# Performance work log

Hardware: AMD Instinct MI355X
Metric: run time of the kernel (lower is better)

## Reference

```python
import jax, jax.numpy as jnp
import numpy as np
import math

D_MODEL = 1024
N_HEADS = 16
D_HEAD = D_MODEL // N_HEADS
B, T = 2, 2048


def setup_inputs() -> dict:
    key = jax.random.key(0)
    ks = jax.random.split(key, 10)
    H = jax.random.normal(ks[0], (B, T, D_MODEL), dtype=jnp.float32)
    key_padding_mask = jnp.zeros((B, T), dtype=bool)
    s = 0.02
    Wq = jax.random.normal(ks[1], (D_MODEL, D_MODEL), dtype=jnp.float32) * s
    bq = jnp.zeros((D_MODEL,), dtype=jnp.float32)
    Wk = jax.random.normal(ks[2], (D_MODEL, D_MODEL), dtype=jnp.float32) * s
    bk = jnp.zeros((D_MODEL,), dtype=jnp.float32)
    Wv = jax.random.normal(ks[3], (D_MODEL, D_MODEL), dtype=jnp.float32) * s
    bv = jnp.zeros((D_MODEL,), dtype=jnp.float32)
    Wo = jax.random.normal(ks[4], (D_MODEL, D_MODEL), dtype=jnp.float32) * s
    bo = jnp.zeros((D_MODEL,), dtype=jnp.float32)
    return {"H": H, "key_padding_mask": key_padding_mask,
            "Wq": Wq, "bq": bq, "Wk": Wk, "bk": bk,
            "Wv": Wv, "bv": bv, "Wo": Wo, "bo": bo}


def _heads(x):
    # [B, T, D] -> [B, nh, T, dh]
    b, t, _ = x.shape
    return x.reshape(b, t, N_HEADS, D_HEAD).transpose(0, 2, 1, 3)


def reference(H, key_padding_mask, Wq, bq, Wk, bk, Wv, bv, Wo, bo):
    b, t, d = H.shape
    q = _heads(H @ Wq.T + bq)
    k = _heads(H @ Wk.T + bk)
    v = _heads(H @ Wv.T + bv)
    scale = 1.0 / math.sqrt(D_HEAD)
    scores = jnp.einsum("bhqd,bhkd->bhqk", q, k) * scale
    # causal: add (mask - 1) * 1e9, as in the torch module (soft -1e9, not -inf)
    idx = jnp.arange(t)
    causal_mask = (idx[None, :] <= idx[:, None]).astype(scores.dtype)
    scores = scores + (causal_mask[None, None, :, :] - 1.0) * 1e9
    # key padding mask: True = masked -> -inf
    scores = jnp.where(key_padding_mask[:, None, None, :], -jnp.inf, scores)
    A = jax.nn.softmax(scores, axis=-1)
    O = jnp.einsum("bhqk,bhkd->bhqd", A, v)
    O = O.transpose(0, 2, 1, 3).reshape(b, t, d)
    return O @ Wo.T + bo
```

## Files before the change

### kernel.cpp

```cpp
#include <hip/hip_runtime.h>
#include <hip/hip_bf16.h>


typedef __bf16 bf16x8 __attribute__((ext_vector_type(8)));
typedef float  f32x4  __attribute__((ext_vector_type(4)));
typedef unsigned short u16x4 __attribute__((ext_vector_type(4)));

#define AS1 __attribute__((address_space(1)))
#define AS3 __attribute__((address_space(3)))

__device__ __forceinline__ void gll16(const void* g, void* l) {
  __builtin_amdgcn_global_load_lds((const AS1 void*)g, (AS3 void*)l, 16, 0, 0);
}

__device__ __forceinline__ unsigned short f2bf(float x) {
  unsigned u = __builtin_bit_cast(unsigned, x);
  u += 0x7fffu + ((u >> 16) & 1u);
  return (unsigned short)(u >> 16);
}

__device__ __forceinline__ unsigned cvtpk(float lo, float hi) {
  unsigned r;
  asm("v_cvt_pk_bf16_f32 %0, %1, %2" : "=v"(r) : "v"(lo), "v"(hi));
  return r;
}

__global__ __launch_bounds__(256) void cvt_kernel(
    const float* __restrict__ H,  const float* __restrict__ Wq,
    const float* __restrict__ Wk, const float* __restrict__ Wv,
    const float* __restrict__ Wo,
    unsigned short* __restrict__ Hb, unsigned short* __restrict__ Wcat,
    unsigned short* __restrict__ Wob)
{
  size_t i = ((size_t)blockIdx.x * 256 + threadIdx.x) * 4;
  const float* s; unsigned short* d;
  if      (i < 4194304u) { s = H  + i;            d = Hb   + i; }
  else if (i < 5242880u) { s = Wq + (i - 4194304); d = Wcat + (i - 4194304); }
  else if (i < 6291456u) { s = Wk + (i - 5242880); d = Wcat + (i - 4194304); }
  else if (i < 7340032u) { s = Wv + (i - 6291456); d = Wcat + (i - 4194304); }
  else                   { s = Wo + (i - 7340032); d = Wob  + (i - 7340032); }
  f32x4 v = *(const f32x4*)s;
  u16x4 o;
  o[0] = f2bf(v[0]); o[1] = f2bf(v[1]); o[2] = f2bf(v[2]); o[3] = f2bf(v[3]);
  *(u16x4*)d = o;
}

__global__ __launch_bounds__(512, 2) void gemm_qkv(
    const unsigned short* __restrict__ A,
    const unsigned short* __restrict__ B,
    const float* __restrict__ b0, const float* __restrict__ b1,
    const float* __restrict__ b2,
    unsigned short* __restrict__ Qb, unsigned short* __restrict__ Kb,
    unsigned short* __restrict__ Vt)
{
  constexpr int K = 1024, NT = 32;
  __shared__ __align__(1024) char smem[131072];
  const int tid = threadIdx.x;
  const int w = tid >> 6, l = tid & 63;
  const int lr = l & 15, lg = l >> 4;
  const int wn = w & 3, wm = w >> 2;

  const int bid = blockIdx.x;
  const int xcd = bid & 7, idx = bid >> 3;
  const int by = (xcd & 3) * 8 + (idx & 7);
  const int bx = (xcd >> 2) * 4 + (idx >> 3);

  const unsigned short* srcB =
      (w < 6) ? B + (size_t)(bx*384 + w*64 + lr) * K + lg*8
              : A + (size_t)(by*128 + (w-6)*64 + lr) * K + lg*8;

  auto stage = [&](int t) {
    const int ring = t & 3;
    const unsigned short* s = srcB + t*32;
    char* d = smem + ring*32768 + w*4096;
#pragma unroll
    for (int i = 0; i < 4; ++i)
      gll16(s + (size_t)i*16*K, d + i*1024);
  };

  f32x4 acc[6][4] = {};

  stage(0); stage(1); stage(2);
  asm volatile("s_waitcnt vmcnt(8)" ::: "memory");
  __builtin_amdgcn_s_barrier();

  for (int t = 0; t < NT; ++t) {
    const char* Wt = smem + (t&3)*32768 + wn*6144;
    const char* Ht = smem + (t&3)*32768 + 24576 + wm*4096;
    bf16x8 wf[6], hf[4];
#pragma unroll
    for (int p = 0; p < 6; ++p)
      wf[p] = *(const bf16x8*)(Wt + p*1024 + l*16);
#pragma unroll
    for (int q = 0; q < 4; ++q)
      hf[q] = *(const bf16x8*)(Ht + q*1024 + l*16);
    if (t + 3 < NT) stage(t + 3);
    __builtin_amdgcn_s_setprio(1);
#pragma unroll
    for (int p = 0; p < 6; ++p)
#pragma unroll
      for (int q = 0; q < 4; ++q)
        acc[p][q] = __builtin_amdgcn_mfma_f32_16x16x32_bf16(wf[p], hf[q], acc[p][q], 0, 0, 0);
    __builtin_amdgcn_s_setprio(0);
    if (t + 3 < NT)      asm volatile("s_waitcnt vmcnt(8)" ::: "memory");
    else if (t + 2 < NT) asm volatile("s_waitcnt vmcnt(4)" ::: "memory");
    else if (t + 1 < NT) asm volatile("s_waitcnt vmcnt(0)" ::: "memory");
    if (t + 1 < NT) __builtin_amdgcn_s_barrier();
  }

  constexpr float CS = 0.125f * 1.44269504088896340736f;
#pragma unroll
  for (int p = 0; p < 6; ++p) {
    const int nG = bx*384 + wn*96 + p*16 + lg*4;
    const int sel = nG >> 10, nl = nG & 1023, h = nl >> 6, dd = nl & 63;
    const float sc = (sel == 0) ? CS : 1.0f;
    const float* bp = (sel == 0) ? b0 : ((sel == 1) ? b1 : b2);
    const f32x4 bias = *(const f32x4*)(bp + nl);
#pragma unroll
    for (int q = 0; q < 4; ++q) {
      const int m = by*128 + wm*64 + q*16 + lr;
      const int bb = m >> 11, tt = m & 2047;
      if (sel < 2) {
        unsigned short* O = sel ? Kb : Qb;
        u16x4 pk;
#pragma unroll
        for (int r = 0; r < 4; ++r) pk[r] = f2bf((acc[p][q][r] + bias[r]) * sc);
        *(u16x4*)(O + ((size_t)(bb*16 + h) * 2048 + tt) * 64 + dd) = pk;
      } else {
#pragma unroll
        for (int r = 0; r < 4; ++r)
          Vt[((size_t)(bb*16 + h) * 64 + dd + r) * 2048 + tt] =
              f2bf(acc[p][q][r] + bias[r]);
      }
    }
  }
}

__global__ __launch_bounds__(512) void gemm_o(
    const unsigned short* __restrict__ A,
    const unsigned short* __restrict__ B,
    float* __restrict__ Cout, const float* __restrict__ bo)
{
  constexpr int K = 1024, NT = 16;
  __shared__ __align__(1024) char smem[81920];
  const int tid = threadIdx.x;
  const int w = tid >> 6, l = tid & 63;
  const int lr = l & 15, lg = l >> 4;
  const int wn = w >> 1, wm = w & 1;

  const int bid = blockIdx.x;
  const int xcd = bid & 7, idx = bid >> 3;
  const int by = xcd * 4 + (idx & 3);
  const int bx = idx >> 2;

  const unsigned short* srcW = B + (size_t)(bx*128 + w*16 + lr) * K + lg*8;
  const unsigned short* srcH = A + (size_t)(by*128 + w*16 + lr) * K + lg*8;

  auto stW = [&](int t) {
    const unsigned short* s = srcW + t*64;
    char* d = smem + (t&1)*16384 + w*2048;
    gll16(s,      d);
    gll16(s + 32, d + 1024);
  };
  auto stH = [&](int t, int ring) {
    const unsigned short* s = srcH + t*64;
    char* d = smem + 32768 + ring*16384 + w*2048;
    gll16(s,      d);
    gll16(s + 32, d + 1024);
  };

  f32x4 acc[2][4] = {};

  stW(0); stH(0, 0); stH(1, 1);
  asm volatile("s_waitcnt vmcnt(2)" ::: "memory");
  __builtin_amdgcn_s_barrier();

  auto tile = [&](int t, int r0, int r2) {
    const char* Wt = smem + (t&1)*16384 + wn*4096;
    const char* Ht = smem + 32768 + r0*16384 + wm*8192;
    bf16x8 wf[2][2], hfa[2][2], hfb[2][2];
#pragma unroll
    for (int p = 0; p < 2; ++p)
#pragma unroll
      for (int kf = 0; kf < 2; ++kf)
        wf[p][kf] = *(const bf16x8*)(Wt + (p*2+kf)*1024 + l*16);
#pragma unroll
    for (int q = 0; q < 2; ++q)
#pragma unroll
      for (int kf = 0; kf < 2; ++kf)
        hfa[q][kf] = *(const bf16x8*)(Ht + (q*2+kf)*1024 + l*16);
    if (t+1 < NT) stW(t+1);
    __builtin_amdgcn_s_barrier();
    __builtin_amdgcn_s_setprio(1);
#pragma unroll
    for (int p = 0; p < 2; ++p)
#pragma unroll
      for (int q = 0; q < 2; ++q)
#pragma unroll
        for (int kf = 0; kf < 2; ++kf)
          acc[p][q] = __builtin_amdgcn_mfma_f32_16x16x32_bf16(wf[p][kf], hfa[q][kf], acc[p][q], 0, 0, 0);
    __builtin_amdgcn_s_setprio(0);
    __builtin_amdgcn_s_barrier();
#pragma unroll
    for (int q = 0; q < 2; ++q)
#pragma unroll
      for (int kf = 0; kf < 2; ++kf)
        hfb[q][kf] = *(const bf16x8*)(Ht + ((q+2)*2+kf)*1024 + l*16);
    if (t+2 < NT) stH(t+2, r2);
    __builtin_amdgcn_s_barrier();
    __builtin_amdgcn_s_setprio(1);
#pragma unroll
    for (int p = 0; p < 2; ++p)
#pragma unroll
      for (int q = 0; q < 2; ++q)
#pragma unroll
        for (int kf = 0; kf < 2; ++kf)
          acc[p][q+2] = __builtin_amdgcn_mfma_f32_16x16x32_bf16(wf[p][kf], hfb[q][kf], acc[p][q+2], 0, 0, 0);
    __builtin_amdgcn_s_setprio(0);
    if (t+2 < NT)      asm volatile("s_waitcnt vmcnt(2)" ::: "memory");
    else if (t+1 < NT) asm volatile("s_waitcnt vmcnt(0)" ::: "memory");
    __builtin_amdgcn_s_barrier();
  };

  int r0 = 0;
  for (int t = 0; t < NT; ++t) {
    int r2 = r0 + 2; if (r2 >= 3) r2 -= 3;
    tile(t, r0, r2);
    ++r0; if (r0 == 3) r0 = 0;
  }

  __syncthreads();
#pragma unroll
  for (int p = 0; p < 2; ++p) {
    const int n0 = wn*32 + p*16 + lg*4;
    const f32x4 bias = *(const f32x4*)(bo + bx*128 + n0);
#pragma unroll
    for (int q = 0; q < 4; ++q) {
      const int m = wm*64 + q*16 + lr;
      *(f32x4*)(smem + m*528 + n0*4) = acc[p][q] + bias;
    }
  }
  __syncthreads();
#pragma unroll
  for (int pass = 0; pass < 8; ++pass) {
    const int m = pass*16 + (tid >> 5), c = tid & 31;
    f32x4 v = *(const f32x4*)(smem + m*528 + c*16);
    *(f32x4*)(Cout + (size_t)(by*128 + m) * 1024 + bx*128 + c*4) = v;
  }
}

__global__ __launch_bounds__(256, 2) void attn_kernel(
    const unsigned short* __restrict__ Qb, const unsigned short* __restrict__ Kb,
    const unsigned short* __restrict__ Vt, unsigned short* __restrict__ AO)
{
  __shared__ char smem[3*16384 + 4*2304];
  const int tid = threadIdx.x;
  const int w  = tid >> 6, l = tid & 63;
  const int lr = l & 15,  lg = l >> 4;
  const int bid = blockIdx.x;
  const int xcd = bid & 7, idx = bid >> 3;
  const int bh = xcd + ((idx & 3) << 3);
  const int pr = idx >> 2;
  const int qtA = pr, qtB = 31 - pr;
  const size_t bh_off = (size_t)bh * 2048 * 64;
  const unsigned short* Qp = Qb + bh_off;
  const unsigned short* Kp = Kb + bh_off;
  const unsigned short* Vp = Vt + bh_off;
  const int qwA = qtA*64 + w*16, qwB = qtB*64 + w*16;

  bf16x8 qfA[2], qfB[2];
#pragma unroll
  for (int kf = 0; kf < 2; ++kf) {
    qfA[kf] = *(const bf16x8*)(Qp + (size_t)(qwA + lr) * 64 + kf*32 + lg*8);
    qfB[kf] = *(const bf16x8*)(Qp + (size_t)(qwB + lr) * 64 + kf*32 + lg*8);
  }

  f32x4 accA[4] = {}, accB[4] = {};
  float mA = -3e38f, lA = 0.f, mB = -3e38f, lB = 0.f;
  char* Pw = smem + 49152 + w * 2304;

  const int nt = qtB + 1;

  auto stage = [&](int t, int b) {
#pragma unroll
    for (int i = 0; i < 2; ++i) {
      const int c = w * 2 + i;
      const int sub = c >> 1, kf = c & 1;
      const int kv0 = t * 64;
      gll16(Kp + (size_t)(kv0 + sub*16 + lr) * 64 + kf*32 + lg*8,
            smem + b * 16384 + c * 1024);
      gll16(Vp + (size_t)(sub*16 + lr) * 2048 + kv0 + kf*32 + lg*8,
            smem + b * 16384 + 8192 + c * 1024);
    }
  };

  auto process = [&](const bf16x8 (&qf)[2], f32x4 (&acc_o)[4], float& m_run,
                     float& l_run, int qw, bool diag, int kv0, int buf) {
    f32x4 accs[4] = {};
    __builtin_amdgcn_s_setprio(1);
#pragma unroll
    for (int kf = 0; kf < 2; ++kf)
#pragma unroll
      for (int kt = 0; kt < 4; ++kt) {
        bf16x8 kfr = *(const bf16x8*)(smem + buf*16384 + (kt*2 + kf)*1024 + l*16);
        accs[kt] = __builtin_amdgcn_mfma_f32_16x16x32_bf16(kfr, qf[kf], accs[kt], 0, 0, 0);
      }
    __builtin_amdgcn_s_setprio(0);

    float s[4][4];
    const int qg = qw + lr;
#pragma unroll
    for (int kt = 0; kt < 4; ++kt)
#pragma unroll
      for (int r = 0; r < 4; ++r) {
        float v = accs[kt][r];
        if (diag) {
          const int kvg = kv0 + kt*16 + lg*4 + r;
          if (kvg > qg) v = -1e30f;
        }
        s[kt][r] = v;
      }

    float mt = s[0][0];
#pragma unroll
    for (int kt = 0; kt < 4; ++kt)
#pragma unroll
      for (int r = 0; r < 4; ++r) mt = fmaxf(mt, s[kt][r]);
    mt = fmaxf(mt, __shfl_xor(mt, 16));
    mt = fmaxf(mt, __shfl_xor(mt, 32));

    if (__any(mt > m_run + 8.f)) {
      const float mnew = fmaxf(m_run, mt);
      const float fac  = __builtin_amdgcn_exp2f(m_run - mnew);
      l_run *= fac;
#pragma unroll
      for (int r = 0; r < 4; ++r) {
        const float fr = __shfl(fac, lg*4 + r);
#pragma unroll
        for (int dt = 0; dt < 4; ++dt) acc_o[dt][r] *= fr;
      }
      m_run = mnew;
    }

    float p[4][4]; float sum = 0.f;
#pragma unroll
    for (int kt = 0; kt < 4; ++kt)
#pragma unroll
      for (int r = 0; r < 4; ++r) {
        const float e = __builtin_amdgcn_exp2f(s[kt][r] - m_run);
        p[kt][r] = e; sum += e;
      }
    sum += __shfl_xor(sum, 16);
    sum += __shfl_xor(sum, 32);
    l_run += sum;

#pragma unroll
    for (int kt = 0; kt < 4; ++kt)
#pragma unroll
      for (int r2 = 0; r2 < 2; ++r2)
        *(unsigned*)(Pw + lr*144 + (kt*16 + lg*4 + r2*2)*2) =
            cvtpk(p[kt][r2*2], p[kt][r2*2+1]);

    __builtin_amdgcn_s_setprio(1);
#pragma unroll
    for (int kf2 = 0; kf2 < 2; ++kf2) {
      bf16x8 pf = *(const bf16x8*)(Pw + lr*144 + kf2*64 + lg*16);
#pragma unroll
      for (int dt = 0; dt < 4; ++dt) {
        bf16x8 vf = *(const bf16x8*)(smem + buf*16384 + 8192 + (dt*2 + kf2)*1024 + l*16);
        acc_o[dt] = __builtin_amdgcn_mfma_f32_16x16x32_bf16(pf, vf, acc_o[dt], 0, 0, 0);
      }
    }
    __builtin_amdgcn_s_setprio(0);
  };

  stage(0, 0); stage(1, 1);
  asm volatile("s_waitcnt vmcnt(4)" ::: "memory");
  __builtin_amdgcn_s_barrier();

  int bcur = 0;
  for (int t = 0; t < nt; ++t) {
    if (t + 2 < nt) {
      int b2 = bcur + 2; if (b2 >= 3) b2 -= 3;
      stage(t + 2, b2);
    }
    process(qfB, accB, mB, lB, qwB, t == qtB, t*64, bcur);
    if (t <= qtA)
      process(qfA, accA, mA, lA, qwA, t == qtA, t*64, bcur);
    if (t + 2 < nt)      asm volatile("s_waitcnt vmcnt(4)" ::: "memory");
    else if (t + 1 < nt) asm volatile("s_waitcnt vmcnt(0)" ::: "memory");
    if (t + 1 < nt) __builtin_amdgcn_s_barrier();
    ++bcur; if (bcur == 3) bcur = 0;
  }

  const int b_ = bh >> 4, h = bh & 15;
#pragma unroll
  for (int r = 0; r < 4; ++r) {
    const float linvB = 1.0f / __shfl(lB, lg*4 + r);
    const int tgB = qwB + lg*4 + r;
    const size_t baseB = ((size_t)(b_*2048 + tgB)) * 1024 + h*64 + lr;
#pragma unroll
    for (int dt = 0; dt < 4; ++dt)
      AO[baseB + dt*16] = f2bf(accB[dt][r] * linvB);
    const float linvA = 1.0f / __shfl(lA, lg*4 + r);
    const int tgA = qwA + lg*4 + r;
    const size_t baseA = ((size_t)(b_*2048 + tgA)) * 1024 + h*64 + lr;
#pragma unroll
    for (int dt = 0; dt < 4; ++dt)
      AO[baseA + dt*16] = f2bf(accA[dt][r] * linvA);
  }
}

extern "C" void kernel_launch(void* const* d_in, const int* in_sizes, int n_in,
                              void* d_out, int out_size, void* d_ws, size_t ws_size,
                              hipStream_t stream) {
  const float* H  = (const float*)d_in[0];
  const float* Wq = (const float*)d_in[2];
  const float* bq = (const float*)d_in[3];
  const float* Wk = (const float*)d_in[4];
  const float* bk = (const float*)d_in[5];
  const float* Wv = (const float*)d_in[6];
  const float* bv = (const float*)d_in[7];
  const float* Wo = (const float*)d_in[8];
  const float* bo = (const float*)d_in[9];

  char* ws = (char*)d_ws;
  unsigned short* Hb   = (unsigned short*)(ws);
  unsigned short* Wcat = (unsigned short*)(ws + 8388608);
  unsigned short* Wob  = (unsigned short*)(ws + 14680064);
  unsigned short* Qb   = (unsigned short*)(ws + 16777216);
  unsigned short* Kb   = (unsigned short*)(ws + 25165824);
  unsigned short* Vt   = (unsigned short*)(ws + 33554432);
  unsigned short* AOb  = (unsigned short*)(ws + 41943040);

  cvt_kernel<<<8192, 256, 0, stream>>>(H, Wq, Wk, Wv, Wo, Hb, Wcat, Wob);
  gemm_qkv<<<256, 512, 0, stream>>>(Hb, Wcat, bq, bk, bv, Qb, Kb, Vt);
  attn_kernel<<<512, 256, 0, stream>>>(Qb, Kb, Vt, AOb);
  gemm_o<<<256, 512, 0, stream>>>(AOb, Wob, (float*)d_out, bo);
}
```

Baseline: 111.7 us.

## Interleave both query tiles' attention steps into one dual-tile pass

While both query tiles are still active, the attention loop now handles them in one interleaved routine. It issues their QK and PV MFMAs side by side from the same K/V fragment loads, and runs their softmax steps together. Each tile gets its own P staging buffer in LDS, so shared memory per block grows. The aim is to cut duplicate LDS reads and give the scheduler more independent work to hide MFMA and exp latency. The cost is higher register pressure under the existing launch bounds, which could cause spills.

```diff
diff --git a/kernel.cpp b/kernel.cpp
--- a/kernel.cpp
+++ b/kernel.cpp
@@ -253,7 +253,7 @@
     const unsigned short* __restrict__ Qb, const unsigned short* __restrict__ Kb,
     const unsigned short* __restrict__ Vt, unsigned short* __restrict__ AO)
 {
-  __shared__ char smem[3*16384 + 4*2304];
+  __shared__ char smem[3*16384 + 8*2304];
   const int tid = threadIdx.x;
   const int w  = tid >> 6, l = tid & 63;
   const int lr = l & 15,  lg = l >> 4;
@@ -277,7 +277,8 @@
 
   f32x4 accA[4] = {}, accB[4] = {};
   float mA = -3e38f, lA = 0.f, mB = -3e38f, lB = 0.f;
-  char* Pw = smem + 49152 + w * 2304;
+  char* PwB = smem + 49152 + w * 2304;
+  char* PwA = smem + 49152 + (w + 4) * 2304;
 
   const int nt = qtB + 1;
 
@@ -294,8 +295,7 @@
     }
   };
 
-  auto process = [&](const bf16x8 (&qf)[2], f32x4 (&acc_o)[4], float& m_run,
-                     float& l_run, int qw, bool diag, int kv0, int buf) {
+  auto process = [&](bool diag, int kv0, int buf) {
     f32x4 accs[4] = {};
     __builtin_amdgcn_s_setprio(1);
 #pragma unroll
@@ -303,12 +303,12 @@
 #pragma unroll
       for (int kt = 0; kt < 4; ++kt) {
         bf16x8 kfr = *(const bf16x8*)(smem + buf*16384 + (kt*2 + kf)*1024 + l*16);
-        accs[kt] = __builtin_amdgcn_mfma_f32_16x16x32_bf16(kfr, qf[kf], accs[kt], 0, 0, 0);
+        accs[kt] = __builtin_amdgcn_mfma_f32_16x16x32_bf16(kfr, qfB[kf], accs[kt], 0, 0, 0);
       }
     __builtin_amdgcn_s_setprio(0);
 
     float s[4][4];
-    const int qg = qw + lr;
+    const int qg = qwB + lr;
 #pragma unroll
     for (int kt = 0; kt < 4; ++kt)
 #pragma unroll
@@ -329,17 +329,17 @@
     mt = fmaxf(mt, __shfl_xor(mt, 16));
     mt = fmaxf(mt, __shfl_xor(mt, 32));
 
-    if (__any(mt > m_run + 8.f)) {
-      const float mnew = fmaxf(m_run, mt);
-      const float fac  = __builtin_amdgcn_exp2f(m_run - mnew);
-      l_run *= fac;
+    if (__any(mt > mB + 8.f)) {
+      const float mnew = fmaxf(mB, mt);
+      const float fac  = __builtin_amdgcn_exp2f(mB - mnew);
+      lB *= fac;
 #pragma unroll
       for (int r = 0; r < 4; ++r) {
         const float fr = __shfl(fac, lg*4 + r);
 #pragma unroll
-        for (int dt = 0; dt < 4; ++dt) acc_o[dt][r] *= fr;
-      }
-      m_run = mnew;
+        for (int dt = 0; dt < 4; ++dt) accB[dt][r] *= fr;
+      }
+      mB = mnew;
     }
 
     float p[4][4]; float sum = 0.f;
@@ -347,28 +347,135 @@
     for (int kt = 0; kt < 4; ++kt)
 #pragma unroll
       for (int r = 0; r < 4; ++r) {
-        const float e = __builtin_amdgcn_exp2f(s[kt][r] - m_run);
+        const float e = __builtin_amdgcn_exp2f(s[kt][r] - mB);
         p[kt][r] = e; sum += e;
       }
     sum += __shfl_xor(sum, 16);
     sum += __shfl_xor(sum, 32);
-    l_run += sum;
+    lB += sum;
 
 #pragma unroll
     for (int kt = 0; kt < 4; ++kt)
 #pragma unroll
       for (int r2 = 0; r2 < 2; ++r2)
-        *(unsigned*)(Pw + lr*144 + (kt*16 + lg*4 + r2*2)*2) =
+        *(unsigned*)(PwB + lr*144 + (kt*16 + lg*4 + r2*2)*2) =
             cvtpk(p[kt][r2*2], p[kt][r2*2+1]);
 
     __builtin_amdgcn_s_setprio(1);
 #pragma unroll
     for (int kf2 = 0; kf2 < 2; ++kf2) {
-      bf16x8 pf = *(const bf16x8*)(Pw + lr*144 + kf2*64 + lg*16);
+      bf16x8 pf = *(const bf16x8*)(PwB + lr*144 + kf2*64 + lg*16);
 #pragma unroll
       for (int dt = 0; dt < 4; ++dt) {
         bf16x8 vf = *(const bf16x8*)(smem + buf*16384 + 8192 + (dt*2 + kf2)*1024 + l*16);
-        acc_o[dt] = __builtin_amdgcn_mfma_f32_16x16x32_bf16(pf, vf, acc_o[dt], 0, 0, 0);
+        accB[dt] = __builtin_amdgcn_mfma_f32_16x16x32_bf16(pf, vf, accB[dt], 0, 0, 0);
+      }
+    }
+    __builtin_amdgcn_s_setprio(0);
+  };
+
+  auto processDual = [&](bool diagA, int kv0, int buf) {
+    f32x4 accsB[4] = {}, accsA[4] = {};
+    __builtin_amdgcn_s_setprio(1);
+#pragma unroll
+    for (int kf = 0; kf < 2; ++kf)
+#pragma unroll
+      for (int kt = 0; kt < 4; ++kt) {
+        bf16x8 kfr = *(const bf16x8*)(smem + buf*16384 + (kt*2 + kf)*1024 + l*16);
+        accsB[kt] = __builtin_amdgcn_mfma_f32_16x16x32_bf16(kfr, qfB[kf], accsB[kt], 0, 0, 0);
+        accsA[kt] = __builtin_amdgcn_mfma_f32_16x16x32_bf16(kfr, qfA[kf], accsA[kt], 0, 0, 0);
+      }
+    __builtin_amdgcn_s_setprio(0);
+
+    float sB[4][4], sA[4][4];
+    const int qgA = qwA + lr;
+#pragma unroll
+    for (int kt = 0; kt < 4; ++kt)
+#pragma unroll
+      for (int r = 0; r < 4; ++r) {
+        sB[kt][r] = accsB[kt][r];
+        float v = accsA[kt][r];
+        if (diagA) {
+          const int kvg = kv0 + kt*16 + lg*4 + r;
+          if (kvg > qgA) v = -1e30f;
+        }
+        sA[kt][r] = v;
+      }
+
+    float mtB = sB[0][0], mtA = sA[0][0];
+#pragma unroll
+    for (int kt = 0; kt < 4; ++kt)
+#pragma unroll
+      for (int r = 0; r < 4; ++r) {
+        mtB = fmaxf(mtB, sB[kt][r]);
+        mtA = fmaxf(mtA, sA[kt][r]);
+      }
+    mtB = fmaxf(mtB, __shfl_xor(mtB, 16));
+    mtA = fmaxf(mtA, __shfl_xor(mtA, 16));
+    mtB = fmaxf(mtB, __shfl_xor(mtB, 32));
+    mtA = fmaxf(mtA, __shfl_xor(mtA, 32));
+
+    if (__any(mtB > mB + 8.f)) {
+      const float mnew = fmaxf(mB, mtB);
+      const float fac  = __builtin_amdgcn_exp2f(mB - mnew);
+      lB *= fac;
+#pragma unroll
+      for (int r = 0; r < 4; ++r) {
+        const float fr = __shfl(fac, lg*4 + r);
+#pragma unroll
+        for (int dt = 0; dt < 4; ++dt) accB[dt][r] *= fr;
+      }
+      mB = mnew;
+    }
+    if (__any(mtA > mA + 8.f)) {
+      const float mnew = fmaxf(mA, mtA);
+      const float fac  = __builtin_amdgcn_exp2f(mA - mnew);
+      lA *= fac;
+#pragma unroll
+      for (int r = 0; r < 4; ++r) {
+        const float fr = __shfl(fac, lg*4 + r);
+#pragma unroll
+        for (int dt = 0; dt < 4; ++dt) accA[dt][r] *= fr;
+      }
+      mA = mnew;
+    }
+
+    float pB[4][4], pA[4][4]; float sumB = 0.f, sumA = 0.f;
+#pragma unroll
+    for (int kt = 0; kt < 4; ++kt)
+#pragma unroll
+      for (int r = 0; r < 4; ++r) {
+        const float eB = __builtin_amdgcn_exp2f(sB[kt][r] - mB);
+        const float eA = __builtin_amdgcn_exp2f(sA[kt][r] - mA);
+        pB[kt][r] = eB; sumB += eB;
+        pA[kt][r] = eA; sumA += eA;
+      }
+    sumB += __shfl_xor(sumB, 16);
+    sumA += __shfl_xor(sumA, 16);
+    sumB += __shfl_xor(sumB, 32);
+    sumA += __shfl_xor(sumA, 32);
+    lB += sumB; lA += sumA;
+
+#pragma unroll
+    for (int kt = 0; kt < 4; ++kt)
+#pragma unroll
+      for (int r2 = 0; r2 < 2; ++r2) {
+        *(unsigned*)(PwB + lr*144 + (kt*16 + lg*4 + r2*2)*2) =
+            cvtpk(pB[kt][r2*2], pB[kt][r2*2+1]);
+        *(unsigned*)(PwA + lr*144 + (kt*16 + lg*4 + r2*2)*2) =
+            cvtpk(pA[kt][r2*2], pA[kt][r2*2+1]);
+      }
+
+    __builtin_amdgcn_s_setprio(1);
+#pragma unroll
+    for (int kf2 = 0; kf2 < 2; ++kf2) {
+      bf16x8 pfB = *(const bf16x8*)(PwB + lr*144 + kf2*64 + lg*16);
+      bf16x8 pfA = *(const bf16x8*)(PwA + lr*144 + kf2*64 + lg*16);
+#pragma unroll
+      for (int dt = 0; dt < 4; ++dt) {
+        bf16x8 vf = *(const bf16x8*)(smem + buf*16384 + 8192 + (dt*2 + kf2)*1024 + l*16);
+        accB[dt] = __builtin_amdgcn_mfma_f32_16x16x32_bf16(pfB, vf, accB[dt], 0, 0, 0);
+        accA[dt] = __builtin_amdgcn_mfma_f32_16x16x32_bf16(pfA, vf, accA[dt], 0, 0, 0);
       }
     }
     __builtin_amdgcn_s_setprio(0);
@@ -384,9 +491,8 @@
       int b2 = bcur + 2; if (b2 >= 3) b2 -= 3;
       stage(t + 2, b2);
     }
-    process(qfB, accB, mB, lB, qwB, t == qtB, t*64, bcur);
-    if (t <= qtA)
-      process(qfA, accA, mA, lA, qwA, t == qtA, t*64, bcur);
+    if (t <= qtA) processDual(t == qtA, t*64, bcur);
+    else          process(t == qtB, t*64, bcur);
     if (t + 2 < nt)      asm volatile("s_waitcnt vmcnt(4)" ::: "memory");
     else if (t + 1 < nt) asm volatile("s_waitcnt vmcnt(0)" ::: "memory");
     if (t + 1 < nt) __builtin_amdgcn_s_barrier();
```

Result: no change. 112.1 us (+0.3%).

## Use 128-wide KV tiles with shared K fragments for both query tiles

Applied to the files above, without the earlier changes.

The attention loop now processes 128 keys per iteration instead of 64, moving from a triple-buffered to a double-buffered LDS schedule. Each K fragment read from LDS feeds the QK^T MFMAs of both paired query tiles, and the causal mask is applied only on the diagonal tile. The P staging buffer uses an XOR swizzle to cut LDS bank conflicts. The aim is fewer barriers and loop iterations and less LDS read traffic, at the cost of more LDS per block, higher register pressure, and less prefetch depth.

```diff
diff --git a/kernel.cpp b/kernel.cpp
--- a/kernel.cpp
+++ b/kernel.cpp
@@ -253,7 +253,7 @@
     const unsigned short* __restrict__ Qb, const unsigned short* __restrict__ Kb,
     const unsigned short* __restrict__ Vt, unsigned short* __restrict__ AO)
 {
-  __shared__ char smem[3*16384 + 4*2304];
+  __shared__ char smem[2*32768 + 4*4096];
   const int tid = threadIdx.x;
   const int w  = tid >> 6, l = tid & 63;
   const int lr = l & 15,  lg = l >> 4;
@@ -277,55 +277,32 @@
 
   f32x4 accA[4] = {}, accB[4] = {};
   float mA = -3e38f, lA = 0.f, mB = -3e38f, lB = 0.f;
-  char* Pw = smem + 49152 + w * 2304;
-
-  const int nt = qtB + 1;
+  char* Pw = smem + 65536 + w * 4096;
+  const int xr = (lr & 7) << 4;
+
+  const int nt = (qtB >> 1) + 1;
+  const int dualEnd = qtA >> 1;
 
   auto stage = [&](int t, int b) {
 #pragma unroll
-    for (int i = 0; i < 2; ++i) {
-      const int c = w * 2 + i;
-      const int sub = c >> 1, kf = c & 1;
-      const int kv0 = t * 64;
-      gll16(Kp + (size_t)(kv0 + sub*16 + lr) * 64 + kf*32 + lg*8,
-            smem + b * 16384 + c * 1024);
-      gll16(Vp + (size_t)(sub*16 + lr) * 2048 + kv0 + kf*32 + lg*8,
-            smem + b * 16384 + 8192 + c * 1024);
-    }
-  };
-
-  auto process = [&](const bf16x8 (&qf)[2], f32x4 (&acc_o)[4], float& m_run,
-                     float& l_run, int qw, bool diag, int kv0, int buf) {
-    f32x4 accs[4] = {};
-    __builtin_amdgcn_s_setprio(1);
-#pragma unroll
-    for (int kf = 0; kf < 2; ++kf)
-#pragma unroll
-      for (int kt = 0; kt < 4; ++kt) {
-        bf16x8 kfr = *(const bf16x8*)(smem + buf*16384 + (kt*2 + kf)*1024 + l*16);
-        accs[kt] = __builtin_amdgcn_mfma_f32_16x16x32_bf16(kfr, qf[kf], accs[kt], 0, 0, 0);
-      }
-    __builtin_amdgcn_s_setprio(0);
-
-    float s[4][4];
-    const int qg = qw + lr;
-#pragma unroll
-    for (int kt = 0; kt < 4; ++kt)
-#pragma unroll
-      for (int r = 0; r < 4; ++r) {
-        float v = accs[kt][r];
-        if (diag) {
-          const int kvg = kv0 + kt*16 + lg*4 + r;
-          if (kvg > qg) v = -1e30f;
-        }
-        s[kt][r] = v;
-      }
-
-    float mt = s[0][0];
-#pragma unroll
-    for (int kt = 0; kt < 4; ++kt)
-#pragma unroll
-      for (int r = 0; r < 4; ++r) mt = fmaxf(mt, s[kt][r]);
+    for (int i = 0; i < 4; ++i) {
+      const int c = w*4 + i;
+      const int kt = c >> 1, kf = c & 1;
+      gll16(Kp + (size_t)(t*128 + kt*16 + lr) * 64 + kf*32 + lg*8,
+            smem + b*32768 + c*1024);
+      const int dt = c >> 2, kf2 = c & 3;
+      gll16(Vp + (size_t)(dt*16 + lr) * 2048 + t*128 + kf2*32 + lg*8,
+            smem + b*32768 + 16384 + c*1024);
+    }
+  };
+
+  auto finish = [&](f32x4 (&a)[8], f32x4 (&acc_o)[4], float& m_run,
+                    float& l_run, int buf) {
+    float mt = a[0][0];
+#pragma unroll
+    for (int kt = 0; kt < 8; ++kt)
+#pragma unroll
+      for (int r = 0; r < 4; ++r) mt = fmaxf(mt, a[kt][r]);
     mt = fmaxf(mt, __shfl_xor(mt, 16));
     mt = fmaxf(mt, __shfl_xor(mt, 32));
 
@@ -342,55 +319,92 @@
       m_run = mnew;
     }
 
-    float p[4][4]; float sum = 0.f;
-#pragma unroll
-    for (int kt = 0; kt < 4; ++kt)
+    float sum = 0.f;
+#pragma unroll
+    for (int kt = 0; kt < 8; ++kt)
 #pragma unroll
       for (int r = 0; r < 4; ++r) {
-        const float e = __builtin_amdgcn_exp2f(s[kt][r] - m_run);
-        p[kt][r] = e; sum += e;
+        const float e = __builtin_amdgcn_exp2f(a[kt][r] - m_run);
+        a[kt][r] = e; sum += e;
       }
     sum += __shfl_xor(sum, 16);
     sum += __shfl_xor(sum, 32);
     l_run += sum;
 
 #pragma unroll
-    for (int kt = 0; kt < 4; ++kt)
+    for (int kt = 0; kt < 8; ++kt)
 #pragma unroll
       for (int r2 = 0; r2 < 2; ++r2)
-        *(unsigned*)(Pw + lr*144 + (kt*16 + lg*4 + r2*2)*2) =
-            cvtpk(p[kt][r2*2], p[kt][r2*2+1]);
+        *(unsigned*)(Pw + lr*256 + ((kt*32 + lg*8 + r2*4) ^ xr)) =
+            cvtpk(a[kt][r2*2], a[kt][r2*2+1]);
 
     __builtin_amdgcn_s_setprio(1);
 #pragma unroll
-    for (int kf2 = 0; kf2 < 2; ++kf2) {
-      bf16x8 pf = *(const bf16x8*)(Pw + lr*144 + kf2*64 + lg*16);
+    for (int kf2 = 0; kf2 < 4; ++kf2) {
+      bf16x8 pf = *(const bf16x8*)(Pw + lr*256 + ((kf2*64 + lg*16) ^ xr));
 #pragma unroll
       for (int dt = 0; dt < 4; ++dt) {
-        bf16x8 vf = *(const bf16x8*)(smem + buf*16384 + 8192 + (dt*2 + kf2)*1024 + l*16);
+        bf16x8 vf = *(const bf16x8*)(smem + buf*32768 + 16384 + (dt*4 + kf2)*1024 + l*16);
         acc_o[dt] = __builtin_amdgcn_mfma_f32_16x16x32_bf16(pf, vf, acc_o[dt], 0, 0, 0);
       }
     }
     __builtin_amdgcn_s_setprio(0);
   };
 
-  stage(0, 0); stage(1, 1);
-  asm volatile("s_waitcnt vmcnt(4)" ::: "memory");
+  auto maskDiag = [&](f32x4 (&a)[8], int qg, int kv0) {
+#pragma unroll
+    for (int kt = 0; kt < 8; ++kt)
+#pragma unroll
+      for (int r = 0; r < 4; ++r) {
+        const int kvg = kv0 + kt*16 + lg*4 + r;
+        if (kvg > qg) a[kt][r] = -1e30f;
+      }
+  };
+
+  stage(0, 0);
+  asm volatile("s_waitcnt vmcnt(0)" ::: "memory");
   __builtin_amdgcn_s_barrier();
 
-  int bcur = 0;
+  int cur = 0;
   for (int t = 0; t < nt; ++t) {
-    if (t + 2 < nt) {
-      int b2 = bcur + 2; if (b2 >= 3) b2 -= 3;
-      stage(t + 2, b2);
-    }
-    process(qfB, accB, mB, lB, qwB, t == qtB, t*64, bcur);
-    if (t <= qtA)
-      process(qfA, accA, mA, lA, qwA, t == qtA, t*64, bcur);
-    if (t + 2 < nt)      asm volatile("s_waitcnt vmcnt(4)" ::: "memory");
-    else if (t + 1 < nt) asm volatile("s_waitcnt vmcnt(0)" ::: "memory");
-    if (t + 1 < nt) __builtin_amdgcn_s_barrier();
-    ++bcur; if (bcur == 3) bcur = 0;
+    if (t + 1 < nt) stage(t + 1, cur ^ 1);
+    const int kv0 = t * 128;
+
+    if (t <= dualEnd) {
+      f32x4 aB[8] = {}, aA[8] = {};
+      __builtin_amdgcn_s_setprio(1);
+#pragma unroll
+      for (int kf = 0; kf < 2; ++kf)
+#pragma unroll
+        for (int kt = 0; kt < 8; ++kt) {
+          bf16x8 kfr = *(const bf16x8*)(smem + cur*32768 + (kt*2 + kf)*1024 + l*16);
+          aB[kt] = __builtin_amdgcn_mfma_f32_16x16x32_bf16(kfr, qfB[kf], aB[kt], 0, 0, 0);
+          aA[kt] = __builtin_amdgcn_mfma_f32_16x16x32_bf16(kfr, qfA[kf], aA[kt], 0, 0, 0);
+        }
+      __builtin_amdgcn_s_setprio(0);
+      if (t == dualEnd) maskDiag(aA, qwA + lr, kv0);
+      finish(aB, accB, mB, lB, cur);
+      finish(aA, accA, mA, lA, cur);
+    } else {
+      f32x4 aB[8] = {};
+      __builtin_amdgcn_s_setprio(1);
+#pragma unroll
+      for (int kf = 0; kf < 2; ++kf)
+#pragma unroll
+        for (int kt = 0; kt < 8; ++kt) {
+          bf16x8 kfr = *(const bf16x8*)(smem + cur*32768 + (kt*2 + kf)*1024 + l*16);
+          aB[kt] = __builtin_amdgcn_mfma_f32_16x16x32_bf16(kfr, qfB[kf], aB[kt], 0, 0, 0);
+        }
+      __builtin_amdgcn_s_setprio(0);
+      if (t == nt - 1) maskDiag(aB, qwB + lr, kv0);
+      finish(aB, accB, mB, lB, cur);
+    }
+
+    if (t + 1 < nt) {
+      asm volatile("s_waitcnt vmcnt(0)" ::: "memory");
+      __builtin_amdgcn_s_barrier();
+    }
+    cur ^= 1;
   }
 
   const int b_ = bh >> 4, h = bh & 15;
```

After: 109.1 us (median of 2 runs). -2.3%, faster.
